# Kernel tuning notes

Measured on AMD Instinct MI355X. Metric: run time of the kernel, lower is better.

Reference implementation:

```python
import jax, jax.numpy as jnp
import numpy as np

N_NODES = 50000
N_EDGES = 800000
N_GRAPHS = 128
IN_CH = 31
HID = 64
EPS = 1e-5


def _glorot(key, shape, scale=0.05):
    return jax.random.normal(key, shape, dtype=jnp.float32) * scale


def setup_inputs() -> dict:
    key = jax.random.key(0)
    ks = jax.random.split(key, 16)
    x = jax.random.normal(ks[0], (N_NODES, IN_CH), dtype=jnp.float32)
    edge_index = jax.random.randint(ks[1], (2, N_EDGES), 0, N_NODES, dtype=jnp.int32)
    batch = jnp.sort(jax.random.randint(ks[2], (N_NODES,), 0, N_GRAPHS, dtype=jnp.int32))
    params = {
        "t": jnp.ones((1,), dtype=jnp.float32),  # shared learnable softmax temperature
        "W1r": _glorot(ks[3], (HID, IN_CH)), "b1": jnp.zeros((HID,), jnp.float32), "W1s": _glorot(ks[4], (HID, IN_CH)),
        "W2r": _glorot(ks[5], (HID, HID)),  "b2": jnp.zeros((HID,), jnp.float32), "W2s": _glorot(ks[6], (HID, HID)),
        "W3r": _glorot(ks[7], (HID, HID)),  "b3": jnp.zeros((HID,), jnp.float32), "W3s": _glorot(ks[8], (HID, HID)),
        "Wl1": _glorot(ks[9], (2 * HID, 3 * HID)), "bl1": jnp.zeros((2 * HID,), jnp.float32),
        "Wl2": _glorot(ks[10], (HID // 2, 2 * HID)), "bl2": jnp.zeros((HID // 2,), jnp.float32),
    }
    return {"x": x, "edge_index": edge_index, "batch": batch, **params}


def _softmax_aggr(m, dst, t, n):
    # segment-softmax over incoming edges, per channel: alpha = softmax(t*m | dst)
    logits = m * t  # [E, C]
    mx = jax.ops.segment_max(logits, dst, num_segments=n)  # [N, C]
    e = jnp.exp(logits - mx[dst])
    denom = jax.ops.segment_sum(e, dst, num_segments=n)
    alpha = e / denom[dst]
    return jax.ops.segment_sum(m * alpha, dst, num_segments=n)  # [N, C]


def _graph_conv(x, src, dst, t, Wr, br, Ws):
    # PyG GraphConv: out = lin_rel(aggr_j x_j) + lin_root(x); lin_root has no bias
    m = x[src]  # gather [E, C]
    aggr = _softmax_aggr(m, dst, t, x.shape[0])
    return aggr @ Wr.T + br + x @ Ws.T


def _instance_norm(x):
    # torch InstanceNorm1d on [N, C] input -> normalize each row over feature dim
    mu = jnp.mean(x, axis=1, keepdims=True)
    var = jnp.mean((x - mu) ** 2, axis=1, keepdims=True)
    return (x - mu) / jnp.sqrt(var + EPS)


def reference(x, edge_index, batch, t, W1r, b1, W1s, W2r, b2, W2s, W3r, b3, W3s, Wl1, bl1, Wl2, bl2):
    src, dst = edge_index[0], edge_index[1]
    x1 = jax.nn.relu(_instance_norm(_graph_conv(x, src, dst, t, W1r, b1, W1s)))
    x2 = jax.nn.relu(_instance_norm(_graph_conv(x1, src, dst, t, W2r, b2, W2s)))
    x3 = jax.nn.relu(_instance_norm(_graph_conv(x2, src, dst, t, W3r, b3, W3s)))
    h1 = jax.ops.segment_max(x1, batch, num_segments=N_GRAPHS)
    h2 = jax.ops.segment_max(x2, batch, num_segments=N_GRAPHS)
    h3 = jax.ops.segment_max(x3, batch, num_segments=N_GRAPHS)
    h = jnp.concatenate([h1, h2, h3], axis=1)  # [G, 3*HID]
    z = jax.nn.relu(h @ Wl1.T + bl1)  # dropout is identity in eval mode
    z = z @ Wl2.T + bl2
    norm = jnp.maximum(jnp.linalg.norm(z, axis=1, keepdims=True), 1e-12)
    return z / norm
```

## Files before the change

### kernel.cpp

```cpp
#include <hip/hip_runtime.h>
#include <hip/hip_fp16.h>

#define N_NODES 50000
#define N_EDGES 800000
#define N_GRAPHS 128
#define IN_CH 31
#define HID 64

typedef __attribute__((ext_vector_type(8))) short short8;
typedef __attribute__((ext_vector_type(8))) unsigned short ushort8;
typedef __attribute__((ext_vector_type(4))) float floatx4;

__device__ inline unsigned f2bf(float f) {
    union { float f; unsigned u; } v; v.f = f;
    unsigned r = v.u + 0x7fff + ((v.u >> 16) & 1);
    return r >> 16;
}
__device__ inline float bf2f(unsigned short u) {
    union { unsigned u; float f; } v; v.u = ((unsigned)u) << 16; return v.f;
}
__device__ inline void pack4(short* p, float4 v) {
    unsigned lo = f2bf(v.x) | (f2bf(v.y) << 16);
    unsigned hi = f2bf(v.z) | (f2bf(v.w) << 16);
    *(uint2*)p = make_uint2(lo, hi);
}
__device__ inline unsigned packEP(float E, float P) {
    __half2 h = __floats2half2_rn(E, P);
    return *(unsigned*)&h;
}
__device__ inline float2 unpackEP(unsigned u) {
    __half2 h = *(__half2*)&u;
    return __half22float2(h);
}

__global__ void prep_kernel(const float* __restrict__ x, const float* __restrict__ tptr,
                            unsigned short* __restrict__ xbf, unsigned* __restrict__ EP0,
                            int nN) {
    int i = blockIdx.x * 256 + threadIdx.x;
    if (i >= nN * 32) return;
    int node = i >> 5, c = i & 31;
    if (c < IN_CH) {
        float xv = x[node * IN_CH + c];
        xbf[node * IN_CH + c] = (unsigned short)f2bf(xv);
        float tval = tptr[0];
        float E = __expf(tval * xv);
        EP0[i] = packEP(E, xv * E);
    } else {
        EP0[i] = 0;
    }
}


#define BKT_SHIFT 7
#define BKT_MAX 512
#define CHUNK 8192
#define CAP 2560

__global__ void bucket_scatter_kernel(const int* __restrict__ src,
                                      const int* __restrict__ dst,
                                      int* __restrict__ bucket_cnt,
                                      unsigned* __restrict__ ebuf, int e, int nb) {
    __shared__ int bins[BKT_MAX];
    __shared__ int base[BKT_MAX];
    __shared__ int lcur[BKT_MAX];
    int tid = threadIdx.x;
    int i0 = blockIdx.x * CHUNK;
    int i1 = i0 + CHUNK; if (i1 > e) i1 = e;
    for (int k = tid; k < nb; k += 256) { bins[k] = 0; lcur[k] = 0; }
    __syncthreads();
    for (int j = i0 + tid; j < i1; j += 256)
        atomicAdd(&bins[dst[j] >> BKT_SHIFT], 1);
    __syncthreads();
    for (int k = tid; k < nb; k += 256)
        if (bins[k]) base[k] = atomicAdd(&bucket_cnt[k], bins[k]);
    __syncthreads();
    for (int j = i0 + tid; j < i1; j += 256) {
        int ss = src[j], dd = dst[j];
        int b = dd >> BKT_SHIFT;
        int p = atomicAdd(&lcur[b], 1);
        ebuf[(size_t)b * CAP + base[b] + p] = (unsigned)ss | ((unsigned)(dd & 127) << 16);
    }
}

__global__ void bucket_csr_kernel(const unsigned* __restrict__ ebuf,
                                  const int* __restrict__ bucket_cnt,
                                  int* __restrict__ row_ptr, int* __restrict__ deg,
                                  int* __restrict__ csr_src, int nN) {
    __shared__ int nh[128];
    __shared__ int s[128];
    __shared__ int ncur[128];
    int tid = threadIdx.x;
    int b = blockIdx.x;
    int cnt = bucket_cnt[b];
    size_t boff = (size_t)b * CAP;
    int node0 = b << BKT_SHIFT;
    if (tid < 128) nh[tid] = 0;
    __syncthreads();
    for (int j = tid; j < cnt; j += 256)
        atomicAdd(&nh[ebuf[boff + j] >> 16], 1);
    __syncthreads();
    int v = (tid < 128) ? nh[tid] : 0;
    if (tid < 128) s[tid] = v;
    __syncthreads();
    for (int off = 1; off < 128; off <<= 1) {
        int u = (tid < 128 && tid >= off) ? s[tid - off] : 0;
        __syncthreads();
        if (tid < 128) s[tid] += u;
        __syncthreads();
    }
    if (tid < 128 && node0 + tid < nN) {
        int excl = (int)boff + s[tid] - v;
        row_ptr[node0 + tid] = excl;
        deg[node0 + tid] = v;
        ncur[tid] = excl;
    }
    __syncthreads();
    for (int j = tid; j < cnt; j += 256) {
        unsigned ed = ebuf[boff + j];
        int pos = atomicAdd(&ncur[ed >> 16], 1);
        csr_src[pos] = (int)(ed & 0xFFFF);
    }
}


template <int C_IN>
__global__ void __launch_bounds__(256, 8) aggr_kernel(
        const unsigned* __restrict__ EP, const unsigned short* __restrict__ xin,
        const int* __restrict__ row_ptr, const int* __restrict__ deg,
        const int* __restrict__ csr_src,
        unsigned short* __restrict__ aRowsB, int n) {
    int w = threadIdx.x >> 6, l = threadIdx.x & 63;
    int d = blockIdx.x * 4 + w;
    if (d >= n) return;
    int beg = __builtin_amdgcn_readfirstlane(row_ptr[d]);
    int end = beg + __builtin_amdgcn_readfirstlane(deg[d]);
    int half = l >> 5;

    if constexpr (C_IN == 64) {
        int co = l & 31;
        float2 num2 = {0.f, 0.f}, den2 = {0.f, 0.f};
        int base = beg;
        for (; base + 64 <= end; base += 64) {
            int sidx = csr_src[base + l];
            #pragma unroll
            for (int j = 0; j < 64; j += 16) {
                uint2 v[8];
                #pragma unroll
                for (int p = 0; p < 8; ++p) {
                    int sa = __builtin_amdgcn_readlane(sidx, j + 2 * p);
                    int sb = __builtin_amdgcn_readlane(sidx, j + 2 * p + 1);
                    int s  = half ? sb : sa;
                    v[p] = *(const uint2*)&EP[(size_t)s * 64 + 2 * co];
                }
                #pragma unroll
                for (int p = 0; p < 8; ++p) {
                    float2 e0 = unpackEP(v[p].x);
                    float2 e1 = unpackEP(v[p].y);
                    den2.x += e0.x; num2.x += e0.y;
                    den2.y += e1.x; num2.y += e1.y;
                }
            }
        }
        int rem = end - base;
        if (rem > 0) {
            int sidx = csr_src[base + ((l < rem) ? l : 0)];
            for (int j = 0; j < rem; j += 16) {
                uint2 v[8];
                #pragma unroll
                for (int p = 0; p < 8; ++p) {
                    int ja = j + 2 * p;     if (ja >= rem) ja = rem - 1;
                    int jb = j + 2 * p + 1; if (jb >= rem) jb = rem - 1;
                    int sa = __builtin_amdgcn_readlane(sidx, ja);
                    int sb = __builtin_amdgcn_readlane(sidx, jb);
                    int s  = half ? sb : sa;
                    v[p] = *(const uint2*)&EP[(size_t)s * 64 + 2 * co];
                }
                #pragma unroll
                for (int p = 0; p < 8; ++p) {
                    float m = (j + 2 * p + half < rem) ? 1.f : 0.f;
                    float2 e0 = unpackEP(v[p].x);
                    float2 e1 = unpackEP(v[p].y);
                    den2.x = fmaf(e0.x, m, den2.x); num2.x = fmaf(e0.y, m, num2.x);
                    den2.y = fmaf(e1.x, m, den2.y); num2.y = fmaf(e1.y, m, num2.y);
                }
            }
        }
        num2.x += __shfl_xor(num2.x, 32);
        num2.y += __shfl_xor(num2.y, 32);
        den2.x += __shfl_xor(den2.x, 32);
        den2.y += __shfl_xor(den2.y, 32);
        float nx = __shfl(num2.x, l >> 1);
        float ny = __shfl(num2.y, l >> 1);
        float dx = __shfl(den2.x, l >> 1);
        float dy = __shfl(den2.y, l >> 1);
        float num = (l & 1) ? ny : nx;
        float den = (l & 1) ? dy : dx;
        float aggr = (end > beg && den > 0.f) ? num / den : 0.f;
        aRowsB[(size_t)d * 64 + l] = (unsigned short)f2bf(aggr);
    } else {
        int ch = l & 31;
        int chc = (ch < C_IN) ? ch : (C_IN - 1);
        float num = 0.f, den = 0.f;
        int base = beg;
        for (; base + 64 <= end; base += 64) {
            int sidx = csr_src[base + l];
            #pragma unroll
            for (int j = 0; j < 64; j += 16) {
                unsigned v[8];
                #pragma unroll
                for (int p = 0; p < 8; ++p) {
                    int sa = __builtin_amdgcn_readlane(sidx, j + 2 * p);
                    int sb = __builtin_amdgcn_readlane(sidx, j + 2 * p + 1);
                    int s  = half ? sb : sa;
                    v[p] = EP[(size_t)s * 32 + chc];
                }
                #pragma unroll
                for (int p = 0; p < 8; ++p) {
                    float2 e = unpackEP(v[p]);
                    den += e.x;
                    num += e.y;
                }
            }
        }
        int rem = end - base;
        if (rem > 0) {
            int sidx = csr_src[base + ((l < rem) ? l : 0)];
            for (int j = 0; j < rem; j += 16) {
                unsigned v[8];
                #pragma unroll
                for (int p = 0; p < 8; ++p) {
                    int ja = j + 2 * p;     if (ja >= rem) ja = rem - 1;
                    int jb = j + 2 * p + 1; if (jb >= rem) jb = rem - 1;
                    int sa = __builtin_amdgcn_readlane(sidx, ja);
                    int sb = __builtin_amdgcn_readlane(sidx, jb);
                    int s  = half ? sb : sa;
                    v[p] = EP[(size_t)s * 32 + chc];
                }
                #pragma unroll
                for (int p = 0; p < 8; ++p) {
                    float m = (j + 2 * p + half < rem) ? 1.f : 0.f;
                    float2 e = unpackEP(v[p]);
                    den = fmaf(e.x, m, den);
                    num = fmaf(e.y, m, num);
                }
            }
        }
        num += __shfl_xor(num, 32);
        den += __shfl_xor(den, 32);
        float aggr = (end > beg && den > 0.f) ? num / den : 0.f;
        unsigned short outv;
        if (l < C_IN)               outv = (unsigned short)f2bf(aggr);
        else if (l < 2 * C_IN)      outv = xin[(size_t)d * C_IN + (l - C_IN)];
        else                        outv = 0;
        aRowsB[(size_t)d * 64 + l] = outv;
    }
}


template <int C_IN, bool WEP>
__global__ void __launch_bounds__(256, 4) transform_kernel(
        const unsigned short* __restrict__ aRowsB, const unsigned short* __restrict__ yprev,
        const int* __restrict__ batch,
        const float* __restrict__ Wr, const float* __restrict__ br,
        const float* __restrict__ Ws, const float* __restrict__ tptr,
        unsigned short* __restrict__ yout, unsigned* __restrict__ EPout,
        float* __restrict__ hmax, int n) {
    constexpr int K_TOT = (C_IN == 64) ? 128 : 64;
    constexpr int KP    = K_TOT + 8;
    constexpr int KS    = K_TOT / 32;
    constexpr int ABSH  = 2 * 64 * KP;
    constexpr int CSH   = 64 * 68 * 2;
    constexpr int SMSH  = (ABSH > CSH) ? ABSH : CSH;

    __shared__ short smem[SMSH];
    short* sA = smem;
    short* sB = smem + 64 * KP;
    float* sC = (float*)smem;

    int tid = threadIdx.x;
    int nb = blockIdx.x * 64;

    if constexpr (C_IN == 64) {
        for (int idx = tid; idx < 64 * 16; idx += 256) {
            int row = idx >> 4, c8 = idx & 15;
            int node = nb + row; if (node >= n) node = n - 1;
            ushort8 v = (c8 < 8) ? ((const ushort8*)(aRowsB + (size_t)node * 64))[c8]
                                 : ((const ushort8*)(yprev + (size_t)node * 64))[c8 - 8];
            *(ushort8*)&sA[row * KP + c8 * 8] = v;
        }
        for (int idx = tid; idx < 64 * 32; idx += 256) {
            int nr = idx >> 5, c4 = idx & 31;
            float4 v = (c4 < 16) ? ((const float4*)(Wr + nr * 64))[c4]
                                 : ((const float4*)(Ws + nr * 64))[c4 - 16];
            pack4(&sB[nr * KP + c4 * 4], v);
        }
    } else {
        for (int idx = tid; idx < 64 * 8; idx += 256) {
            int row = idx >> 3, c8 = idx & 7;
            int node = nb + row; if (node >= n) node = n - 1;
            ushort8 v = ((const ushort8*)(aRowsB + (size_t)node * 64))[c8];
            *(ushort8*)&sA[row * KP + c8 * 8] = v;
        }
        for (int idx = tid; idx < 64 * 64; idx += 256) {
            int nr = idx >> 6, k = idx & 63;
            float v = (k < C_IN) ? Wr[nr * C_IN + k]
                    : (k < 2 * C_IN) ? Ws[nr * C_IN + (k - C_IN)] : 0.f;
            sB[nr * KP + k] = (short)f2bf(v);
        }
    }
    __syncthreads();

    int w = tid >> 6, l = tid & 63;
    int m = l & 15;
    int q = l >> 4;
    floatx4 acc[4] = {{0.f,0.f,0.f,0.f},{0.f,0.f,0.f,0.f},
                      {0.f,0.f,0.f,0.f},{0.f,0.f,0.f,0.f}};
    const short* aBase = &sA[(w * 16 + m) * KP + q * 8];
    #pragma unroll 2
    for (int s = 0; s < KS; ++s) {
        short8 af = *(const short8*)(aBase + s * 32);
        #pragma unroll
        for (int t = 0; t < 4; ++t) {
            short8 bf = *(const short8*)&sB[(t * 16 + m) * KP + q * 8 + s * 32];
            acc[t] = __builtin_amdgcn_mfma_f32_16x16x32_bf16(af, bf, acc[t], 0, 0, 0);
        }
    }

    __syncthreads();
    #pragma unroll
    for (int t = 0; t < 4; ++t)
        #pragma unroll
        for (int r = 0; r < 4; ++r)
            sC[(w * 16 + q * 4 + r) * 68 + t * 16 + m] = acc[t][r];
    __syncthreads();

    float bias = br[l];
    float tval = 0.f;
    if constexpr (WEP) tval = tptr[0];
    int gcur = -1;
    float rmax = 0.f;
    for (int i = 0; i < 16; ++i) {
        int j = w * 16 + i;
        int d = nb + j;
        if (d < n) {
            float a = sC[j * 68 + l] + bias;
            float s = a;
            for (int off = 32; off > 0; off >>= 1) s += __shfl_xor(s, off);
            float mu = s * (1.0f / 64.0f);
            float dc = a - mu;
            float s2 = dc * dc;
            for (int off = 32; off > 0; off >>= 1) s2 += __shfl_xor(s2, off);
            float var = s2 * (1.0f / 64.0f);
            float y = dc * rsqrtf(var + 1e-5f);
            y = fmaxf(y, 0.f);
            yout[(size_t)d * 64 + l] = (unsigned short)f2bf(y);
            if constexpr (WEP) {
                float E = __expf(tval * y);
                EPout[(size_t)d * 64 + l] = packEP(E, y * E);
            }
            int g = __builtin_amdgcn_readfirstlane(batch[d]);
            if (g != gcur) {
                if (gcur >= 0)
                    atomicMax((int*)&hmax[gcur * 64 + l], __float_as_int(rmax));
                gcur = g;
                rmax = 0.f;
            }
            rmax = fmaxf(rmax, y);
        }
    }
    if (gcur >= 0)
        atomicMax((int*)&hmax[gcur * 64 + l], __float_as_int(rmax));
}


__global__ void mlp_kernel(const float* __restrict__ h,
                           const float* __restrict__ Wl1, const float* __restrict__ bl1,
                           const float* __restrict__ Wl2, const float* __restrict__ bl2,
                           float* __restrict__ out) {
    __shared__ float hrow[192];
    __shared__ float z1[128];
    __shared__ float z2[32];
    __shared__ float snorm;
    int g = blockIdx.x, tid = threadIdx.x;
    if (tid < 64) {
        hrow[tid]       = h[0 * N_GRAPHS * 64 + g * 64 + tid];
        hrow[64 + tid]  = h[1 * N_GRAPHS * 64 + g * 64 + tid];
        hrow[128 + tid] = h[2 * N_GRAPHS * 64 + g * 64 + tid];
    }
    __syncthreads();
    float acc = bl1[tid];
    #pragma unroll 8
    for (int c = 0; c < 192; ++c) acc = fmaf(hrow[c], Wl1[tid * 192 + c], acc);
    z1[tid] = fmaxf(acc, 0.f);
    __syncthreads();
    if (tid < 32) {
        float a2 = bl2[tid];
        #pragma unroll 8
        for (int c = 0; c < 128; ++c) a2 = fmaf(z1[c], Wl2[tid * 128 + c], a2);
        z2[tid] = a2;
    }
    __syncthreads();
    if (tid == 0) {
        float ss = 0.f;
        for (int i = 0; i < 32; ++i) ss += z2[i] * z2[i];
        snorm = fmaxf(sqrtf(ss), 1e-12f);
    }
    __syncthreads();
    if (tid < 32) out[g * 32 + tid] = z2[tid] / snorm;
}


extern "C" void kernel_launch(void* const* d_in, const int* in_sizes, int n_in,
                              void* d_out, int out_size, void* d_ws, size_t ws_size,
                              hipStream_t stream) {
    const float* x   = (const float*)d_in[0];
    const int* eidx  = (const int*)d_in[1];
    const int* batch = (const int*)d_in[2];
    const float* t   = (const float*)d_in[3];
    const float* W1r = (const float*)d_in[4];
    const float* b1  = (const float*)d_in[5];
    const float* W1s = (const float*)d_in[6];
    const float* W2r = (const float*)d_in[7];
    const float* b2  = (const float*)d_in[8];
    const float* W2s = (const float*)d_in[9];
    const float* W3r = (const float*)d_in[10];
    const float* b3  = (const float*)d_in[11];
    const float* W3s = (const float*)d_in[12];
    const float* Wl1 = (const float*)d_in[13];
    const float* bl1 = (const float*)d_in[14];
    const float* Wl2 = (const float*)d_in[15];
    const float* bl2 = (const float*)d_in[16];
    float* out = (float*)d_out;

    const int nE = in_sizes[1] / 2;
    const int nN = in_sizes[2];
    const int* src = eidx;
    const int* dst = eidx + nE;
    const int nb = (nN + 127) >> BKT_SHIFT;

    char* ws = (char*)d_ws;
    size_t off = 0;
    auto alloc = [&](size_t bytes) {
        char* p = ws + off;
        off = (off + bytes + 255) & ~(size_t)255;
        return p;
    };
    int*            bucket_cnt = (int*)alloc((size_t)BKT_MAX * 4);
    float*          h          = (float*)alloc((size_t)3 * N_GRAPHS * 64 * 4);
    int*            row_ptr    = (int*)alloc((size_t)nN * 4);
    int*            deg        = (int*)alloc((size_t)nN * 4);
    unsigned*       ebuf       = (unsigned*)alloc((size_t)nb * CAP * 4);
    int*            csr_src    = (int*)alloc((size_t)nb * CAP * 4);
    unsigned short* xbf        = (unsigned short*)alloc((size_t)nN * IN_CH * 2);
    unsigned*       EP0        = (unsigned*)alloc((size_t)nN * 32 * 4);
    unsigned*       EPbuf      = (unsigned*)alloc((size_t)nN * 64 * 4);
    unsigned short* aRowsB     = (unsigned short*)alloc((size_t)nN * 64 * 2);
    unsigned short* yAb        = (unsigned short*)alloc((size_t)nN * 64 * 2);
    unsigned short* yBb        = (unsigned short*)alloc((size_t)nN * 64 * 2);

    const int nbChunk = (nE + CHUNK - 1) / CHUNK;

    hipMemsetAsync(bucket_cnt, 0,
                   (char*)(h + 3 * N_GRAPHS * 64) - (char*)bucket_cnt, stream);
    prep_kernel<<<(nN * 32 + 255) / 256, 256, 0, stream>>>(x, t, xbf, EP0, nN);
    bucket_scatter_kernel<<<nbChunk, 256, 0, stream>>>(src, dst, bucket_cnt, ebuf, nE, nb);
    bucket_csr_kernel<<<nb, 256, 0, stream>>>(ebuf, bucket_cnt, row_ptr, deg, csr_src, nN);

    const int nbA = (nN + 3) / 4;
    const int nbT = (nN + 63) / 64;

    aggr_kernel<IN_CH><<<nbA, 256, 0, stream>>>(EP0, xbf, row_ptr, deg, csr_src, aRowsB, nN);
    transform_kernel<IN_CH, true><<<nbT, 256, 0, stream>>>(
        aRowsB, nullptr, batch, W1r, b1, W1s, t, yAb, EPbuf, h + 0 * N_GRAPHS * 64, nN);

    aggr_kernel<HID><<<nbA, 256, 0, stream>>>(EPbuf, nullptr, row_ptr, deg, csr_src, aRowsB, nN);
    transform_kernel<HID, true><<<nbT, 256, 0, stream>>>(
        aRowsB, yAb, batch, W2r, b2, W2s, t, yBb, EPbuf, h + 1 * N_GRAPHS * 64, nN);

    aggr_kernel<HID><<<nbA, 256, 0, stream>>>(EPbuf, nullptr, row_ptr, deg, csr_src, aRowsB, nN);
    transform_kernel<HID, false><<<nbT, 256, 0, stream>>>(
        aRowsB, yBb, batch, W3r, b3, W3s, t, yAb, nullptr, h + 2 * N_GRAPHS * 64, nN);

    mlp_kernel<<<N_GRAPHS, 128, 0, stream>>>(h, Wl1, bl1, Wl2, bl2, out);
}
```

Measured before the change: 278.6 us.

## Fuse neighbor aggregation into transform kernel, staging aggregated rows in LDS

Merges the per-node softmax aggregation kernel into the per-layer GEMM/norm kernel. Each wave now aggregates 16 destination nodes directly into shared memory before the MFMA transform. This removes the aRowsB global round trip and three kernel launches. EP buffers are now ping-ponged, and the last layer skips writing y. In exchange, the gather phase runs with fewer, larger blocks (64 nodes per block, occupancy hint 4), which may expose more latency in the irregular gathers.

```diff
diff --git a/kernel.cpp b/kernel.cpp
--- a/kernel.cpp
+++ b/kernel.cpp
@@ -15,9 +15,6 @@
     union { float f; unsigned u; } v; v.f = f;
     unsigned r = v.u + 0x7fff + ((v.u >> 16) & 1);
     return r >> 16;
-}
-__device__ inline float bf2f(unsigned short u) {
-    union { unsigned u; float f; } v; v.u = ((unsigned)u) << 16; return v.f;
 }
 __device__ inline void pack4(short* p, float4 v) {
     unsigned lo = f2bf(v.x) | (f2bf(v.y) << 16);
@@ -123,144 +120,12 @@
 }
 
 
-template <int C_IN>
-__global__ void __launch_bounds__(256, 8) aggr_kernel(
-        const unsigned* __restrict__ EP, const unsigned short* __restrict__ xin,
+template <int C_IN, bool WEP>
+__global__ void __launch_bounds__(256, 4) layer_kernel(
+        const unsigned* __restrict__ EP, const unsigned short* __restrict__ xbf,
+        const unsigned short* __restrict__ yprev,
         const int* __restrict__ row_ptr, const int* __restrict__ deg,
-        const int* __restrict__ csr_src,
-        unsigned short* __restrict__ aRowsB, int n) {
-    int w = threadIdx.x >> 6, l = threadIdx.x & 63;
-    int d = blockIdx.x * 4 + w;
-    if (d >= n) return;
-    int beg = __builtin_amdgcn_readfirstlane(row_ptr[d]);
-    int end = beg + __builtin_amdgcn_readfirstlane(deg[d]);
-    int half = l >> 5;
-
-    if constexpr (C_IN == 64) {
-        int co = l & 31;
-        float2 num2 = {0.f, 0.f}, den2 = {0.f, 0.f};
-        int base = beg;
-        for (; base + 64 <= end; base += 64) {
-            int sidx = csr_src[base + l];
-            #pragma unroll
-            for (int j = 0; j < 64; j += 16) {
-                uint2 v[8];
-                #pragma unroll
-                for (int p = 0; p < 8; ++p) {
-                    int sa = __builtin_amdgcn_readlane(sidx, j + 2 * p);
-                    int sb = __builtin_amdgcn_readlane(sidx, j + 2 * p + 1);
-                    int s  = half ? sb : sa;
-                    v[p] = *(const uint2*)&EP[(size_t)s * 64 + 2 * co];
-                }
-                #pragma unroll
-                for (int p = 0; p < 8; ++p) {
-                    float2 e0 = unpackEP(v[p].x);
-                    float2 e1 = unpackEP(v[p].y);
-                    den2.x += e0.x; num2.x += e0.y;
-                    den2.y += e1.x; num2.y += e1.y;
-                }
-            }
-        }
-        int rem = end - base;
-        if (rem > 0) {
-            int sidx = csr_src[base + ((l < rem) ? l : 0)];
-            for (int j = 0; j < rem; j += 16) {
-                uint2 v[8];
-                #pragma unroll
-                for (int p = 0; p < 8; ++p) {
-                    int ja = j + 2 * p;     if (ja >= rem) ja = rem - 1;
-                    int jb = j + 2 * p + 1; if (jb >= rem) jb = rem - 1;
-                    int sa = __builtin_amdgcn_readlane(sidx, ja);
-                    int sb = __builtin_amdgcn_readlane(sidx, jb);
-                    int s  = half ? sb : sa;
-                    v[p] = *(const uint2*)&EP[(size_t)s * 64 + 2 * co];
-                }
-                #pragma unroll
-                for (int p = 0; p < 8; ++p) {
-                    float m = (j + 2 * p + half < rem) ? 1.f : 0.f;
-                    float2 e0 = unpackEP(v[p].x);
-                    float2 e1 = unpackEP(v[p].y);
-                    den2.x = fmaf(e0.x, m, den2.x); num2.x = fmaf(e0.y, m, num2.x);
-                    den2.y = fmaf(e1.x, m, den2.y); num2.y = fmaf(e1.y, m, num2.y);
-                }
-            }
-        }
-        num2.x += __shfl_xor(num2.x, 32);
-        num2.y += __shfl_xor(num2.y, 32);
-        den2.x += __shfl_xor(den2.x, 32);
-        den2.y += __shfl_xor(den2.y, 32);
-        float nx = __shfl(num2.x, l >> 1);
-        float ny = __shfl(num2.y, l >> 1);
-        float dx = __shfl(den2.x, l >> 1);
-        float dy = __shfl(den2.y, l >> 1);
-        float num = (l & 1) ? ny : nx;
-        float den = (l & 1) ? dy : dx;
-        float aggr = (end > beg && den > 0.f) ? num / den : 0.f;
-        aRowsB[(size_t)d * 64 + l] = (unsigned short)f2bf(aggr);
-    } else {
-        int ch = l & 31;
-        int chc = (ch < C_IN) ? ch : (C_IN - 1);
-        float num = 0.f, den = 0.f;
-        int base = beg;
-        for (; base + 64 <= end; base += 64) {
-            int sidx = csr_src[base + l];
-            #pragma unroll
-            for (int j = 0; j < 64; j += 16) {
-                unsigned v[8];
-                #pragma unroll
-                for (int p = 0; p < 8; ++p) {
-                    int sa = __builtin_amdgcn_readlane(sidx, j + 2 * p);
-                    int sb = __builtin_amdgcn_readlane(sidx, j + 2 * p + 1);
-                    int s  = half ? sb : sa;
-                    v[p] = EP[(size_t)s * 32 + chc];
-                }
-                #pragma unroll
-                for (int p = 0; p < 8; ++p) {
-                    float2 e = unpackEP(v[p]);
-                    den += e.x;
-                    num += e.y;
-                }
-            }
-        }
-        int rem = end - base;
-        if (rem > 0) {
-            int sidx = csr_src[base + ((l < rem) ? l : 0)];
-            for (int j = 0; j < rem; j += 16) {
-                unsigned v[8];
-                #pragma unroll
-                for (int p = 0; p < 8; ++p) {
-                    int ja = j + 2 * p;     if (ja >= rem) ja = rem - 1;
-                    int jb = j + 2 * p + 1; if (jb >= rem) jb = rem - 1;
-                    int sa = __builtin_amdgcn_readlane(sidx, ja);
-                    int sb = __builtin_amdgcn_readlane(sidx, jb);
-                    int s  = half ? sb : sa;
-                    v[p] = EP[(size_t)s * 32 + chc];
-                }
-                #pragma unroll
-                for (int p = 0; p < 8; ++p) {
-                    float m = (j + 2 * p + half < rem) ? 1.f : 0.f;
-                    float2 e = unpackEP(v[p]);
-                    den = fmaf(e.x, m, den);
-                    num = fmaf(e.y, m, num);
-                }
-            }
-        }
-        num += __shfl_xor(num, 32);
-        den += __shfl_xor(den, 32);
-        float aggr = (end > beg && den > 0.f) ? num / den : 0.f;
-        unsigned short outv;
-        if (l < C_IN)               outv = (unsigned short)f2bf(aggr);
-        else if (l < 2 * C_IN)      outv = xin[(size_t)d * C_IN + (l - C_IN)];
-        else                        outv = 0;
-        aRowsB[(size_t)d * 64 + l] = outv;
-    }
-}
-
-
-template <int C_IN, bool WEP>
-__global__ void __launch_bounds__(256, 4) transform_kernel(
-        const unsigned short* __restrict__ aRowsB, const unsigned short* __restrict__ yprev,
-        const int* __restrict__ batch,
+        const int* __restrict__ csr_src, const int* __restrict__ batch,
         const float* __restrict__ Wr, const float* __restrict__ br,
         const float* __restrict__ Ws, const float* __restrict__ tptr,
         unsigned short* __restrict__ yout, unsigned* __restrict__ EPout,
@@ -279,15 +144,9 @@
 
     int tid = threadIdx.x;
     int nb = blockIdx.x * 64;
+    int w = tid >> 6, l = tid & 63;
 
     if constexpr (C_IN == 64) {
-        for (int idx = tid; idx < 64 * 16; idx += 256) {
-            int row = idx >> 4, c8 = idx & 15;
-            int node = nb + row; if (node >= n) node = n - 1;
-            ushort8 v = (c8 < 8) ? ((const ushort8*)(aRowsB + (size_t)node * 64))[c8]
-                                 : ((const ushort8*)(yprev + (size_t)node * 64))[c8 - 8];
-            *(ushort8*)&sA[row * KP + c8 * 8] = v;
-        }
         for (int idx = tid; idx < 64 * 32; idx += 256) {
             int nr = idx >> 5, c4 = idx & 31;
             float4 v = (c4 < 16) ? ((const float4*)(Wr + nr * 64))[c4]
@@ -295,12 +154,6 @@
             pack4(&sB[nr * KP + c4 * 4], v);
         }
     } else {
-        for (int idx = tid; idx < 64 * 8; idx += 256) {
-            int row = idx >> 3, c8 = idx & 7;
-            int node = nb + row; if (node >= n) node = n - 1;
-            ushort8 v = ((const ushort8*)(aRowsB + (size_t)node * 64))[c8];
-            *(ushort8*)&sA[row * KP + c8 * 8] = v;
-        }
         for (int idx = tid; idx < 64 * 64; idx += 256) {
             int nr = idx >> 6, k = idx & 63;
             float v = (k < C_IN) ? Wr[nr * C_IN + k]
@@ -308,9 +161,140 @@
             sB[nr * KP + k] = (short)f2bf(v);
         }
     }
-    __syncthreads();
-
-    int w = tid >> 6, l = tid & 63;
+
+    int half = l >> 5;
+    for (int i = 0; i < 16; ++i) {
+        int row = w * 16 + i;
+        int d = nb + row;
+        bool valid = (d < n);
+        int dd = valid ? d : (n - 1);
+        int beg = __builtin_amdgcn_readfirstlane(row_ptr[dd]);
+        int dg  = valid ? __builtin_amdgcn_readfirstlane(deg[dd]) : 0;
+        int end = beg + dg;
+
+        if constexpr (C_IN == 64) {
+            int co = l & 31;
+            float2 num2 = {0.f, 0.f}, den2 = {0.f, 0.f};
+            int base = beg;
+            for (; base + 64 <= end; base += 64) {
+                int sidx = csr_src[base + l];
+                #pragma unroll
+                for (int j = 0; j < 64; j += 16) {
+                    uint2 v[8];
+                    #pragma unroll
+                    for (int p = 0; p < 8; ++p) {
+                        int sa = __builtin_amdgcn_readlane(sidx, j + 2 * p);
+                        int sb = __builtin_amdgcn_readlane(sidx, j + 2 * p + 1);
+                        int s  = half ? sb : sa;
+                        v[p] = *(const uint2*)&EP[(size_t)s * 64 + 2 * co];
+                    }
+                    #pragma unroll
+                    for (int p = 0; p < 8; ++p) {
+                        float2 e0 = unpackEP(v[p].x);
+                        float2 e1 = unpackEP(v[p].y);
+                        den2.x += e0.x; num2.x += e0.y;
+                        den2.y += e1.x; num2.y += e1.y;
+                    }
+                }
+            }
+            int rem = end - base;
+            if (rem > 0) {
+                int sidx = csr_src[base + ((l < rem) ? l : 0)];
+                for (int j = 0; j < rem; j += 16) {
+                    uint2 v[8];
+                    #pragma unroll
+                    for (int p = 0; p < 8; ++p) {
+                        int ja = j + 2 * p;     if (ja >= rem) ja = rem - 1;
+                        int jb = j + 2 * p + 1; if (jb >= rem) jb = rem - 1;
+                        int sa = __builtin_amdgcn_readlane(sidx, ja);
+                        int sb = __builtin_amdgcn_readlane(sidx, jb);
+                        int s  = half ? sb : sa;
+                        v[p] = *(const uint2*)&EP[(size_t)s * 64 + 2 * co];
+                    }
+                    #pragma unroll
+                    for (int p = 0; p < 8; ++p) {
+                        float m = (j + 2 * p + half < rem) ? 1.f : 0.f;
+                        float2 e0 = unpackEP(v[p].x);
+                        float2 e1 = unpackEP(v[p].y);
+                        den2.x = fmaf(e0.x, m, den2.x); num2.x = fmaf(e0.y, m, num2.x);
+                        den2.y = fmaf(e1.x, m, den2.y); num2.y = fmaf(e1.y, m, num2.y);
+                    }
+                }
+            }
+            num2.x += __shfl_xor(num2.x, 32);
+            num2.y += __shfl_xor(num2.y, 32);
+            den2.x += __shfl_xor(den2.x, 32);
+            den2.y += __shfl_xor(den2.y, 32);
+            float nx = __shfl(num2.x, l >> 1);
+            float ny = __shfl(num2.y, l >> 1);
+            float dx = __shfl(den2.x, l >> 1);
+            float dy = __shfl(den2.y, l >> 1);
+            float num = (l & 1) ? ny : nx;
+            float den = (l & 1) ? dy : dx;
+            float aggr = (dg > 0 && den > 0.f) ? num / den : 0.f;
+            sA[row * KP + l] = (short)f2bf(aggr);
+            unsigned short yv = valid ? yprev[(size_t)d * 64 + l] : 0;
+            sA[row * KP + 64 + l] = (short)yv;
+        } else {
+            int ch = l & 31;
+            int chc = (ch < C_IN) ? ch : (C_IN - 1);
+            float num = 0.f, den = 0.f;
+            int base = beg;
+            for (; base + 64 <= end; base += 64) {
+                int sidx = csr_src[base + l];
+                #pragma unroll
+                for (int j = 0; j < 64; j += 16) {
+                    unsigned v[8];
+                    #pragma unroll
+                    for (int p = 0; p < 8; ++p) {
+                        int sa = __builtin_amdgcn_readlane(sidx, j + 2 * p);
+                        int sb = __builtin_amdgcn_readlane(sidx, j + 2 * p + 1);
+                        int s  = half ? sb : sa;
+                        v[p] = EP[(size_t)s * 32 + chc];
+                    }
+                    #pragma unroll
+                    for (int p = 0; p < 8; ++p) {
+                        float2 e = unpackEP(v[p]);
+                        den += e.x;
+                        num += e.y;
+                    }
+                }
+            }
+            int rem = end - base;
+            if (rem > 0) {
+                int sidx = csr_src[base + ((l < rem) ? l : 0)];
+                for (int j = 0; j < rem; j += 16) {
+                    unsigned v[8];
+                    #pragma unroll
+                    for (int p = 0; p < 8; ++p) {
+                        int ja = j + 2 * p;     if (ja >= rem) ja = rem - 1;
+                        int jb = j + 2 * p + 1; if (jb >= rem) jb = rem - 1;
+                        int sa = __builtin_amdgcn_readlane(sidx, ja);
+                        int sb = __builtin_amdgcn_readlane(sidx, jb);
+                        int s  = half ? sb : sa;
+                        v[p] = EP[(size_t)s * 32 + chc];
+                    }
+                    #pragma unroll
+                    for (int p = 0; p < 8; ++p) {
+                        float m = (j + 2 * p + half < rem) ? 1.f : 0.f;
+                        float2 e = unpackEP(v[p]);
+                        den = fmaf(e.x, m, den);
+                        num = fmaf(e.y, m, num);
+                    }
+                }
+            }
+            num += __shfl_xor(num, 32);
+            den += __shfl_xor(den, 32);
+            float aggr = (dg > 0 && den > 0.f) ? num / den : 0.f;
+            unsigned short outv;
+            if (l < C_IN)          outv = (unsigned short)f2bf(aggr);
+            else if (l < 2 * C_IN) outv = valid ? xbf[(size_t)d * C_IN + (l - C_IN)] : 0;
+            else                   outv = 0;
+            sA[row * KP + l] = (short)outv;
+        }
+    }
+    __syncthreads();
+
     int m = l & 15;
     int q = l >> 4;
     floatx4 acc[4] = {{0.f,0.f,0.f,0.f},{0.f,0.f,0.f,0.f},
@@ -353,8 +337,8 @@
             float var = s2 * (1.0f / 64.0f);
             float y = dc * rsqrtf(var + 1e-5f);
             y = fmaxf(y, 0.f);
-            yout[(size_t)d * 64 + l] = (unsigned short)f2bf(y);
             if constexpr (WEP) {
+                yout[(size_t)d * 64 + l] = (unsigned short)f2bf(y);
                 float E = __expf(tval * y);
                 EPout[(size_t)d * 64 + l] = packEP(E, y * E);
             }
@@ -453,8 +437,8 @@
     int*            csr_src    = (int*)alloc((size_t)nb * CAP * 4);
     unsigned short* xbf        = (unsigned short*)alloc((size_t)nN * IN_CH * 2);
     unsigned*       EP0        = (unsigned*)alloc((size_t)nN * 32 * 4);
-    unsigned*       EPbuf      = (unsigned*)alloc((size_t)nN * 64 * 4);
-    unsigned short* aRowsB     = (unsigned short*)alloc((size_t)nN * 64 * 2);
+    unsigned*       EPA        = (unsigned*)alloc((size_t)nN * 64 * 4);
+    unsigned*       EPB        = (unsigned*)alloc((size_t)nN * 64 * 4);
     unsigned short* yAb        = (unsigned short*)alloc((size_t)nN * 64 * 2);
     unsigned short* yBb        = (unsigned short*)alloc((size_t)nN * 64 * 2);
 
@@ -466,20 +450,19 @@
     bucket_scatter_kernel<<<nbChunk, 256, 0, stream>>>(src, dst, bucket_cnt, ebuf, nE, nb);
     bucket_csr_kernel<<<nb, 256, 0, stream>>>(ebuf, bucket_cnt, row_ptr, deg, csr_src, nN);
 
-    const int nbA = (nN + 3) / 4;
     const int nbT = (nN + 63) / 64;
 
-    aggr_kernel<IN_CH><<<nbA, 256, 0, stream>>>(EP0, xbf, row_ptr, deg, csr_src, aRowsB, nN);
-    transform_kernel<IN_CH, true><<<nbT, 256, 0, stream>>>(
-        aRowsB, nullptr, batch, W1r, b1, W1s, t, yAb, EPbuf, h + 0 * N_GRAPHS * 64, nN);
-
-    aggr_kernel<HID><<<nbA, 256, 0, stream>>>(EPbuf, nullptr, row_ptr, deg, csr_src, aRowsB, nN);
-    transform_kernel<HID, true><<<nbT, 256, 0, stream>>>(
-        aRowsB, yAb, batch, W2r, b2, W2s, t, yBb, EPbuf, h + 1 * N_GRAPHS * 64, nN);
-
-    aggr_kernel<HID><<<nbA, 256, 0, stream>>>(EPbuf, nullptr, row_ptr, deg, csr_src, aRowsB, nN);
-    transform_kernel<HID, false><<<nbT, 256, 0, stream>>>(
-        aRowsB, yBb, batch, W3r, b3, W3s, t, yAb, nullptr, h + 2 * N_GRAPHS * 64, nN);
+    layer_kernel<IN_CH, true><<<nbT, 256, 0, stream>>>(
+        EP0, xbf, nullptr, row_ptr, deg, csr_src, batch,
+        W1r, b1, W1s, t, yAb, EPA, h + 0 * N_GRAPHS * 64, nN);
+
+    layer_kernel<HID, true><<<nbT, 256, 0, stream>>>(
+        EPA, nullptr, yAb, row_ptr, deg, csr_src, batch,
+        W2r, b2, W2s, t, yBb, EPB, h + 1 * N_GRAPHS * 64, nN);
+
+    layer_kernel<HID, false><<<nbT, 256, 0, stream>>>(
+        EPB, nullptr, yBb, row_ptr, deg, csr_src, batch,
+        W3r, b3, W3s, t, nullptr, nullptr, h + 2 * N_GRAPHS * 64, nN);
 
     mlp_kernel<<<N_GRAPHS, 128, 0, stream>>>(h, Wl1, bl1, Wl2, bl2, out);
 }
```

Measured after the change: 331.4 us. +19.0%, slower.

## Widen aggregation gathers to 16-byte loads with four edges per wave step

Applied to the files above, without the earlier changes.

The aggregation kernel now assigns 16 lanes per edge, so each wave gathers four edges at once with uint4 loads for the 64-channel layers and uint2 loads for the 31-channel layer, where the old code used two edges with narrower loads. Cross-lane reductions gain an extra xor-shuffle stage, and the loops are kept rolled to limit register pressure. Separately, the last layer's transform no longer writes its node activations, since nothing reads them. This is meant to cut the number of memory instructions in the gather-bound aggregation, at the cost of more lane-select logic and more shuffles.

```diff
diff --git a/kernel.cpp b/kernel.cpp
--- a/kernel.cpp
+++ b/kernel.cpp
@@ -15,9 +15,6 @@
     union { float f; unsigned u; } v; v.f = f;
     unsigned r = v.u + 0x7fff + ((v.u >> 16) & 1);
     return r >> 16;
-}
-__device__ inline float bf2f(unsigned short u) {
-    union { unsigned u; float f; } v; v.u = ((unsigned)u) << 16; return v.f;
 }
 __device__ inline void pack4(short* p, float4 v) {
     unsigned lo = f2bf(v.x) | (f2bf(v.y) << 16);
@@ -125,7 +122,7 @@
 
 template <int C_IN>
 __global__ void __launch_bounds__(256, 8) aggr_kernel(
-        const unsigned* __restrict__ EP, const unsigned short* __restrict__ xin,
+        const unsigned* __restrict__ EP, const unsigned short* __restrict__ xbf,
         const int* __restrict__ row_ptr, const int* __restrict__ deg,
         const int* __restrict__ csr_src,
         unsigned short* __restrict__ aRowsB, int n) {
@@ -133,24 +130,114 @@
     int d = blockIdx.x * 4 + w;
     if (d >= n) return;
     int beg = __builtin_amdgcn_readfirstlane(row_ptr[d]);
-    int end = beg + __builtin_amdgcn_readfirstlane(deg[d]);
-    int half = l >> 5;
+    int dg  = __builtin_amdgcn_readfirstlane(deg[d]);
+    int end = beg + dg;
+    int q4  = l >> 4;
+    int m16 = l & 15;
 
     if constexpr (C_IN == 64) {
-        int co = l & 31;
+        float4 num4 = {0.f,0.f,0.f,0.f}, den4 = {0.f,0.f,0.f,0.f};
+        int base = beg;
+        #pragma unroll 1
+        for (; base + 64 <= end; base += 64) {
+            int sidx = csr_src[base + l];
+            #pragma unroll 1
+            for (int j = 0; j < 64; j += 32) {
+                uint4 v[8];
+                #pragma unroll
+                for (int p = 0; p < 8; ++p) {
+                    int e = j + 4 * p;
+                    int s0 = __builtin_amdgcn_readlane(sidx, e);
+                    int s1 = __builtin_amdgcn_readlane(sidx, e + 1);
+                    int s2 = __builtin_amdgcn_readlane(sidx, e + 2);
+                    int s3 = __builtin_amdgcn_readlane(sidx, e + 3);
+                    int s = (q4 == 0) ? s0 : (q4 == 1) ? s1 : (q4 == 2) ? s2 : s3;
+                    v[p] = *(const uint4*)&EP[(size_t)s * 64 + 4 * m16];
+                }
+                #pragma unroll
+                for (int p = 0; p < 8; ++p) {
+                    float2 e0 = unpackEP(v[p].x);
+                    float2 e1 = unpackEP(v[p].y);
+                    float2 e2 = unpackEP(v[p].z);
+                    float2 e3 = unpackEP(v[p].w);
+                    den4.x += e0.x; num4.x += e0.y;
+                    den4.y += e1.x; num4.y += e1.y;
+                    den4.z += e2.x; num4.z += e2.y;
+                    den4.w += e3.x; num4.w += e3.y;
+                }
+            }
+        }
+        int rem = end - base;
+        if (rem > 0) {
+            int sidx = csr_src[base + ((l < rem) ? l : 0)];
+            for (int j = 0; j < rem; j += 32) {
+                uint4 v[8];
+                float msk[8];
+                #pragma unroll
+                for (int p = 0; p < 8; ++p) {
+                    int e = j + 4 * p;
+                    int c0 = e;     if (c0 >= rem) c0 = rem - 1;
+                    int c1 = e + 1; if (c1 >= rem) c1 = rem - 1;
+                    int c2 = e + 2; if (c2 >= rem) c2 = rem - 1;
+                    int c3 = e + 3; if (c3 >= rem) c3 = rem - 1;
+                    int s0 = __builtin_amdgcn_readlane(sidx, c0);
+                    int s1 = __builtin_amdgcn_readlane(sidx, c1);
+                    int s2 = __builtin_amdgcn_readlane(sidx, c2);
+                    int s3 = __builtin_amdgcn_readlane(sidx, c3);
+                    int s = (q4 == 0) ? s0 : (q4 == 1) ? s1 : (q4 == 2) ? s2 : s3;
+                    msk[p] = (e + q4 < rem) ? 1.f : 0.f;
+                    v[p] = *(const uint4*)&EP[(size_t)s * 64 + 4 * m16];
+                }
+                #pragma unroll
+                for (int p = 0; p < 8; ++p) {
+                    float m = msk[p];
+                    float2 e0 = unpackEP(v[p].x);
+                    float2 e1 = unpackEP(v[p].y);
+                    float2 e2 = unpackEP(v[p].z);
+                    float2 e3 = unpackEP(v[p].w);
+                    den4.x = fmaf(e0.x, m, den4.x); num4.x = fmaf(e0.y, m, num4.x);
+                    den4.y = fmaf(e1.x, m, den4.y); num4.y = fmaf(e1.y, m, num4.y);
+                    den4.z = fmaf(e2.x, m, den4.z); num4.z = fmaf(e2.y, m, num4.z);
+                    den4.w = fmaf(e3.x, m, den4.w); num4.w = fmaf(e3.y, m, num4.w);
+                }
+            }
+        }
+        num4.x += __shfl_xor(num4.x, 16); num4.x += __shfl_xor(num4.x, 32);
+        num4.y += __shfl_xor(num4.y, 16); num4.y += __shfl_xor(num4.y, 32);
+        num4.z += __shfl_xor(num4.z, 16); num4.z += __shfl_xor(num4.z, 32);
+        num4.w += __shfl_xor(num4.w, 16); num4.w += __shfl_xor(num4.w, 32);
+        den4.x += __shfl_xor(den4.x, 16); den4.x += __shfl_xor(den4.x, 32);
+        den4.y += __shfl_xor(den4.y, 16); den4.y += __shfl_xor(den4.y, 32);
+        den4.z += __shfl_xor(den4.z, 16); den4.z += __shfl_xor(den4.z, 32);
+        den4.w += __shfl_xor(den4.w, 16); den4.w += __shfl_xor(den4.w, 32);
+        int srcl = l >> 2;
+        float n0 = __shfl(num4.x, srcl), n1 = __shfl(num4.y, srcl);
+        float n2 = __shfl(num4.z, srcl), n3 = __shfl(num4.w, srcl);
+        float d0 = __shfl(den4.x, srcl), d1 = __shfl(den4.y, srcl);
+        float d2 = __shfl(den4.z, srcl), d3 = __shfl(den4.w, srcl);
+        int k = l & 3;
+        float num = (k == 0) ? n0 : (k == 1) ? n1 : (k == 2) ? n2 : n3;
+        float den = (k == 0) ? d0 : (k == 1) ? d1 : (k == 2) ? d2 : d3;
+        float aggr = (dg > 0 && den > 0.f) ? num / den : 0.f;
+        aRowsB[(size_t)d * 64 + l] = (unsigned short)f2bf(aggr);
+    } else {
         float2 num2 = {0.f, 0.f}, den2 = {0.f, 0.f};
         int base = beg;
+        #pragma unroll 1
         for (; base + 64 <= end; base += 64) {
             int sidx = csr_src[base + l];
-            #pragma unroll
-            for (int j = 0; j < 64; j += 16) {
+            #pragma unroll 1
+            for (int j = 0; j < 64; j += 32) {
                 uint2 v[8];
                 #pragma unroll
                 for (int p = 0; p < 8; ++p) {
-                    int sa = __builtin_amdgcn_readlane(sidx, j + 2 * p);
-                    int sb = __builtin_amdgcn_readlane(sidx, j + 2 * p + 1);
-                    int s  = half ? sb : sa;
-                    v[p] = *(const uint2*)&EP[(size_t)s * 64 + 2 * co];
+                    int e = j + 4 * p;
+                    int s0 = __builtin_amdgcn_readlane(sidx, e);
+                    int s1 = __builtin_amdgcn_readlane(sidx, e + 1);
+                    int s2 = __builtin_amdgcn_readlane(sidx, e + 2);
+                    int s3 = __builtin_amdgcn_readlane(sidx, e + 3);
+                    int s = (q4 == 0) ? s0 : (q4 == 1) ? s1 : (q4 == 2) ? s2 : s3;
+                    v[p] = *(const uint2*)&EP[(size_t)s * 32 + 2 * m16];
                 }
                 #pragma unroll
                 for (int p = 0; p < 8; ++p) {
@@ -164,20 +251,27 @@
         int rem = end - base;
         if (rem > 0) {
             int sidx = csr_src[base + ((l < rem) ? l : 0)];
-            for (int j = 0; j < rem; j += 16) {
+            for (int j = 0; j < rem; j += 32) {
                 uint2 v[8];
-                #pragma unroll
-                for (int p = 0; p < 8; ++p) {
-                    int ja = j + 2 * p;     if (ja >= rem) ja = rem - 1;
-                    int jb = j + 2 * p + 1; if (jb >= rem) jb = rem - 1;
-                    int sa = __builtin_amdgcn_readlane(sidx, ja);
-                    int sb = __builtin_amdgcn_readlane(sidx, jb);
-                    int s  = half ? sb : sa;
-                    v[p] = *(const uint2*)&EP[(size_t)s * 64 + 2 * co];
-                }
-                #pragma unroll
-                for (int p = 0; p < 8; ++p) {
-                    float m = (j + 2 * p + half < rem) ? 1.f : 0.f;
+                float msk[8];
+                #pragma unroll
+                for (int p = 0; p < 8; ++p) {
+                    int e = j + 4 * p;
+                    int c0 = e;     if (c0 >= rem) c0 = rem - 1;
+                    int c1 = e + 1; if (c1 >= rem) c1 = rem - 1;
+                    int c2 = e + 2; if (c2 >= rem) c2 = rem - 1;
+                    int c3 = e + 3; if (c3 >= rem) c3 = rem - 1;
+                    int s0 = __builtin_amdgcn_readlane(sidx, c0);
+                    int s1 = __builtin_amdgcn_readlane(sidx, c1);
+                    int s2 = __builtin_amdgcn_readlane(sidx, c2);
+                    int s3 = __builtin_amdgcn_readlane(sidx, c3);
+                    int s = (q4 == 0) ? s0 : (q4 == 1) ? s1 : (q4 == 2) ? s2 : s3;
+                    msk[p] = (e + q4 < rem) ? 1.f : 0.f;
+                    v[p] = *(const uint2*)&EP[(size_t)s * 32 + 2 * m16];
+                }
+                #pragma unroll
+                for (int p = 0; p < 8; ++p) {
+                    float m = msk[p];
                     float2 e0 = unpackEP(v[p].x);
                     float2 e1 = unpackEP(v[p].y);
                     den2.x = fmaf(e0.x, m, den2.x); num2.x = fmaf(e0.y, m, num2.x);
@@ -185,73 +279,20 @@
                 }
             }
         }
-        num2.x += __shfl_xor(num2.x, 32);
-        num2.y += __shfl_xor(num2.y, 32);
-        den2.x += __shfl_xor(den2.x, 32);
-        den2.y += __shfl_xor(den2.y, 32);
-        float nx = __shfl(num2.x, l >> 1);
-        float ny = __shfl(num2.y, l >> 1);
-        float dx = __shfl(den2.x, l >> 1);
-        float dy = __shfl(den2.y, l >> 1);
+        num2.x += __shfl_xor(num2.x, 16); num2.x += __shfl_xor(num2.x, 32);
+        num2.y += __shfl_xor(num2.y, 16); num2.y += __shfl_xor(num2.y, 32);
+        den2.x += __shfl_xor(den2.x, 16); den2.x += __shfl_xor(den2.x, 32);
+        den2.y += __shfl_xor(den2.y, 16); den2.y += __shfl_xor(den2.y, 32);
+        int srcl = l >> 1;
+        float nx = __shfl(num2.x, srcl), ny = __shfl(num2.y, srcl);
+        float dx = __shfl(den2.x, srcl), dy = __shfl(den2.y, srcl);
         float num = (l & 1) ? ny : nx;
         float den = (l & 1) ? dy : dx;
-        float aggr = (end > beg && den > 0.f) ? num / den : 0.f;
-        aRowsB[(size_t)d * 64 + l] = (unsigned short)f2bf(aggr);
-    } else {
-        int ch = l & 31;
-        int chc = (ch < C_IN) ? ch : (C_IN - 1);
-        float num = 0.f, den = 0.f;
-        int base = beg;
-        for (; base + 64 <= end; base += 64) {
-            int sidx = csr_src[base + l];
-            #pragma unroll
-            for (int j = 0; j < 64; j += 16) {
-                unsigned v[8];
-                #pragma unroll
-                for (int p = 0; p < 8; ++p) {
-                    int sa = __builtin_amdgcn_readlane(sidx, j + 2 * p);
-                    int sb = __builtin_amdgcn_readlane(sidx, j + 2 * p + 1);
-                    int s  = half ? sb : sa;
-                    v[p] = EP[(size_t)s * 32 + chc];
-                }
-                #pragma unroll
-                for (int p = 0; p < 8; ++p) {
-                    float2 e = unpackEP(v[p]);
-                    den += e.x;
-                    num += e.y;
-                }
-            }
-        }
-        int rem = end - base;
-        if (rem > 0) {
-            int sidx = csr_src[base + ((l < rem) ? l : 0)];
-            for (int j = 0; j < rem; j += 16) {
-                unsigned v[8];
-                #pragma unroll
-                for (int p = 0; p < 8; ++p) {
-                    int ja = j + 2 * p;     if (ja >= rem) ja = rem - 1;
-                    int jb = j + 2 * p + 1; if (jb >= rem) jb = rem - 1;
-                    int sa = __builtin_amdgcn_readlane(sidx, ja);
-                    int sb = __builtin_amdgcn_readlane(sidx, jb);
-                    int s  = half ? sb : sa;
-                    v[p] = EP[(size_t)s * 32 + chc];
-                }
-                #pragma unroll
-                for (int p = 0; p < 8; ++p) {
-                    float m = (j + 2 * p + half < rem) ? 1.f : 0.f;
-                    float2 e = unpackEP(v[p]);
-                    den = fmaf(e.x, m, den);
-                    num = fmaf(e.y, m, num);
-                }
-            }
-        }
-        num += __shfl_xor(num, 32);
-        den += __shfl_xor(den, 32);
-        float aggr = (end > beg && den > 0.f) ? num / den : 0.f;
+        float aggr = (dg > 0 && den > 0.f) ? num / den : 0.f;
         unsigned short outv;
-        if (l < C_IN)               outv = (unsigned short)f2bf(aggr);
-        else if (l < 2 * C_IN)      outv = xin[(size_t)d * C_IN + (l - C_IN)];
-        else                        outv = 0;
+        if (l < C_IN)          outv = (unsigned short)f2bf(aggr);
+        else if (l < 2 * C_IN) outv = xbf[(size_t)d * C_IN + (l - C_IN)];
+        else                   outv = 0;
         aRowsB[(size_t)d * 64 + l] = outv;
     }
 }
@@ -353,8 +394,8 @@
             float var = s2 * (1.0f / 64.0f);
             float y = dc * rsqrtf(var + 1e-5f);
             y = fmaxf(y, 0.f);
-            yout[(size_t)d * 64 + l] = (unsigned short)f2bf(y);
             if constexpr (WEP) {
+                yout[(size_t)d * 64 + l] = (unsigned short)f2bf(y);
                 float E = __expf(tval * y);
                 EPout[(size_t)d * 64 + l] = packEP(E, y * E);
             }
@@ -479,7 +520,7 @@
 
     aggr_kernel<HID><<<nbA, 256, 0, stream>>>(EPbuf, nullptr, row_ptr, deg, csr_src, aRowsB, nN);
     transform_kernel<HID, false><<<nbT, 256, 0, stream>>>(
-        aRowsB, yBb, batch, W3r, b3, W3s, t, yAb, nullptr, h + 2 * N_GRAPHS * 64, nN);
+        aRowsB, yBb, batch, W3r, b3, W3s, t, nullptr, nullptr, h + 2 * N_GRAPHS * 64, nN);
 
     mlp_kernel<<<N_GRAPHS, 128, 0, stream>>>(h, Wl1, bl1, Wl2, bl2, out);
 }
```

Measured after the change: 284.2 us. 1.02x slower.
